# Kernel optimization log

Measured on AMD Instinct MI355X. Metric: run time of the kernel, lower is better.

The kernel has to match this reference:

```python
import jax, jax.numpy as jnp
import numpy as np

TOPK = 13
NUM_CLASSES = 80
ALPHA = 1.0
BETA = 6.0
EPS = 1e-9
CIOU_EPS = 1e-7
IMG = 640
STRIDES = (8, 16, 32)


def _make_anchors():
    anchors = []
    for s in STRIDES:
        n = IMG // s
        xs = (np.arange(n, dtype=np.float32) + 0.5) * s
        gy, gx = np.meshgrid(xs, xs, indexing='ij')
        anchors.append(np.stack([gx.ravel(), gy.ravel()], axis=1))
    return jnp.asarray(np.concatenate(anchors, axis=0))  # (8400, 2)


def setup_inputs() -> dict:
    key = jax.random.key(0)
    k1, k2, k3, k4, k5, k6 = jax.random.split(key, 6)
    B, M, A, C = 16, 64, 8400, 80
    anchor_tensor = _make_anchors()                                   # (A,2)
    pd_scores = jax.random.uniform(k1, (B, A, C), dtype=jnp.float32)  # post-sigmoid scores
    # decoded boxes: anchor +/- positive ltrb distances -> valid x0y0x1y1
    d = jax.random.uniform(k2, (B, A, 4), minval=2.0, maxval=120.0, dtype=jnp.float32)
    anc = anchor_tensor[None]
    pd_boxes = jnp.concatenate([anc - d[..., :2], anc + d[..., 2:]], axis=-1)
    centers = jax.random.uniform(k3, (B, M, 2), minval=16.0, maxval=624.0, dtype=jnp.float32)
    wh = jax.random.uniform(k4, (B, M, 2), minval=8.0, maxval=160.0, dtype=jnp.float32)
    gt_boxes = jnp.concatenate([centers - wh / 2, centers + wh / 2], axis=-1)
    gt_classes = jax.random.randint(k5, (B, M, 1), 0, C, dtype=jnp.int64)
    nvalid = jax.random.randint(k6, (B, 1), 8, M + 1)
    gt_mask = (jnp.arange(M)[None, :] < nvalid)[..., None]            # (B,M,1) bool
    return {"pd_scores": pd_scores, "pd_boxes": pd_boxes, "anchor_tensor": anchor_tensor,
            "gt_classes": gt_classes, "gt_boxes": gt_boxes, "gt_mask": gt_mask}


def boxes_ciou(b1, b2):
    """CIoU between broadcast-compatible x0y0x1y1 boxes; returns same leading shape."""
    b1x1, b1y1, b1x2, b1y2 = b1[..., 0], b1[..., 1], b1[..., 2], b1[..., 3]
    b2x1, b2y1, b2x2, b2y2 = b2[..., 0], b2[..., 1], b2[..., 2], b2[..., 3]
    w1, h1 = b1x2 - b1x1, b1y2 - b1y1 + CIOU_EPS
    w2, h2 = b2x2 - b2x1, b2y2 - b2y1 + CIOU_EPS
    inter = (jnp.minimum(b1x2, b2x2) - jnp.maximum(b1x1, b2x1)).clip(0) * \
            (jnp.minimum(b1y2, b2y2) - jnp.maximum(b1y1, b2y1)).clip(0)
    union = w1 * h1 + w2 * h2 - inter + CIOU_EPS
    iou = inter / union
    cw = jnp.maximum(b1x2, b2x2) - jnp.minimum(b1x1, b2x1)
    ch = jnp.maximum(b1y2, b2y2) - jnp.minimum(b1y1, b2y1)
    c2 = cw * cw + ch * ch + CIOU_EPS
    rho2 = ((b2x1 + b2x2 - b1x1 - b1x2) ** 2 + (b2y1 + b2y2 - b1y1 - b1y2) ** 2) / 4.0
    v = (4.0 / (jnp.pi ** 2)) * (jnp.arctan(w2 / h2) - jnp.arctan(w1 / h1)) ** 2
    alpha = jax.lax.stop_gradient(v / (v - iou + (1.0 + CIOU_EPS)))
    return iou - (rho2 / c2 + v * alpha)


def reference(pd_scores, pd_boxes, anchor_tensor, gt_classes, gt_boxes, gt_mask):
    B, A, C = pd_scores.shape
    M = gt_boxes.shape[1]

    # --- anchors inside GT boxes -> (B, M, A) mask ---
    lt = gt_boxes[:, :, None, :2]                     # (B,M,1,2)
    rb = gt_boxes[:, :, None, 2:]
    anc = anchor_tensor[None, None]                   # (1,1,A,2)
    deltas = jnp.concatenate([anc - lt, rb - anc], axis=-1)   # (B,M,A,4)
    anchors_mask = deltas.min(axis=-1) > 1e-9          # (B,M,A)

    # --- alignment metric ---
    cls = gt_classes[..., 0]                           # (B,M) int
    bi = jnp.arange(B)[:, None, None]
    ai = jnp.arange(A)[None, None, :]
    scores = pd_scores[bi, ai, cls[:, :, None]]        # (B,M,A)
    scores = jnp.where(anchors_mask, scores, 0.0)
    ious = boxes_ciou(gt_boxes[:, :, None, :], pd_boxes[:, None, :, :]).clip(0)
    ious = jnp.where(anchors_mask, ious, 0.0)          # (B,M,A)
    align_metric = scores ** ALPHA * ious ** BETA

    # --- top-k candidate selection with duplicate-count filtering ---
    _, topk_idx = jax.lax.top_k(align_metric, TOPK)    # (B,M,K)
    topk_idx = jnp.where(gt_mask, topk_idx, 0)         # invalid GT -> index 0 (as torch masked_fill)
    mi = jnp.arange(M)[None, :, None]
    counts = jnp.zeros((B, M, A), jnp.int32).at[bi, mi, topk_idx].add(1)
    topk_mask = counts == 1                            # counts>1 zeroed, bool()
    positive_mask = anchors_mask & topk_mask

    # --- filter duplicate anchor assignments (keep highest-IoU GT) ---
    fg = positive_mask.sum(axis=-2)                    # (B,A)
    dup = (fg > 1)[:, None, :]                         # (B,1,A)
    max_iou_idx = jnp.argmax(ious, axis=1)             # (B,A)
    max_iou_mask = jnp.arange(M)[None, :, None] == max_iou_idx[:, None, :]
    positive_mask = jnp.where(dup, max_iou_mask, positive_mask)
    fg = positive_mask.sum(axis=-2)
    target_indices = jnp.argmax(positive_mask, axis=-2)  # (B,A) first-True index
    fg_mask = fg > 0                                     # (B,A) bool

    # --- gather targets ---
    target_boxes = jnp.take_along_axis(gt_boxes, target_indices[:, :, None], axis=1)  # (B,A,4)
    tc = jnp.take_along_axis(cls, target_indices, axis=1).clip(0)                      # (B,A)
    target_scores = jax.nn.one_hot(tc, C, dtype=pd_scores.dtype)
    target_scores = jnp.where(fg_mask[..., None], target_scores, 0.0)

    # --- normalize scores by aligned metric ---
    align_metric = align_metric * positive_mask
    max_align = align_metric.max(axis=-1, keepdims=True)            # (B,M,1)
    max_ious = (ious * positive_mask).max(axis=-1, keepdims=True)   # (B,M,1)
    norm = (align_metric * max_ious / (max_align + EPS)).max(axis=-2)[..., None]  # (B,A,1)
    target_scores = target_scores * norm
    return target_scores, target_boxes, fg_mask
```

## Files before the change

kernel.cpp:

```cpp
#include <hip/hip_runtime.h>
#include <math.h>

#define B_N 16
#define M_N 64
#define A_N 8400
#define C_N 80
#define TOPK_N 13
#define LIST_CAP 640
#define MAIN_CAP (LIST_CAP - TOPK_N)
#define MSK_W 263

__device__ __forceinline__ float2 anchor_xy(int a) {
    int i, j; float s;
    if (a < 6400)      { i = a / 80;            j = a - i * 80; s = 8.f;  }
    else if (a < 8000) { int k = a - 6400; i = k / 40; j = k - i * 40; s = 16.f; }
    else               { int k = a - 8000; i = k / 20; j = k - i * 20; s = 32.f; }
    return make_float2(((float)j + 0.5f) * s, ((float)i + 0.5f) * s);
}

__device__ __forceinline__ float ciou_clip(
    float gx1, float gy1, float gx2, float gy2,
    float w1h1, float atg,
    float px1, float py1, float px2, float py2)
{
    float w2 = px2 - px1;
    float h2 = py2 - py1 + 1e-7f;
    float iw = fminf(gx2, px2) - fmaxf(gx1, px1);
    float ih = fminf(gy2, py2) - fmaxf(gy1, py1);
    float inter = fmaxf(iw, 0.f) * fmaxf(ih, 0.f);
    float uni = w1h1 + w2 * h2 - inter + 1e-7f;
    float iou = inter / uni;
    float cw = fmaxf(gx2, px2) - fminf(gx1, px1);
    float ch = fmaxf(gy2, py2) - fminf(gy1, py1);
    float c2 = cw * cw + ch * ch + 1e-7f;
    float dx = px1 + px2 - gx1 - gx2;
    float dy = py1 + py2 - gy1 - gy2;
    float rho2 = (dx * dx + dy * dy) * 0.25f;
    float dat = atanf(w2 / h2) - atg;
    float v = 0.40528473456935109f * (dat * dat);
    float alpha = v / (v - iou + 1.0000001f);
    return fmaxf(iou - (rho2 / c2 + v * alpha), 0.f);
}

__global__ __launch_bounds__(256) void k_topk(
    const float* __restrict__ pd_scores, const float* __restrict__ pd_boxes,
    const int* __restrict__ gt_classes, const float* __restrict__ gt_boxes,
    const int* __restrict__ gt_mask, unsigned long long* __restrict__ pick)
{
    int bm = blockIdx.x;
    if (!gt_mask[bm]) return;
    int b = bm >> 6, m = bm & 63;
    __shared__ unsigned long long s_list[LIST_CAP];
    __shared__ unsigned int s_msk[MSK_W];
    __shared__ unsigned long long s_key[TOPK_N];
    __shared__ int s_n;
    int tid = threadIdx.x;
    int lane = tid & 63;

    const float* g = gt_boxes + (size_t)bm * 4;
    float gx1 = g[0], gy1 = g[1], gx2 = g[2], gy2 = g[3];
    float w1 = gx2 - gx1, h1 = gy2 - gy1 + 1e-7f;
    float w1h1 = w1 * h1;
    float atg = atanf(w1 / h1);

    if (tid == 0) s_n = 0;
    if (tid < TOPK_N) s_key[tid] = 0ull;
    __syncthreads();

    for (int a = tid; a < A_N; a += 256) {
        float2 an = anchor_xy(a);
        float dmin = fminf(fminf(an.x - gx1, an.y - gy1),
                           fminf(gx2 - an.x, gy2 - an.y));
        bool inb = dmin > 1e-9f;
        unsigned long long mk = __ballot(inb);
        if (lane == 0)       s_msk[a >> 5] = (unsigned int)mk;
        else if (lane == 32) s_msk[a >> 5] = (unsigned int)(mk >> 32);
        if (inb) {
            int ldr = __ffsll(mk) - 1;
            int base = 0;
            if (lane == ldr) base = atomicAdd(&s_n, __popcll(mk));
            base = __shfl(base, ldr, 64);
            int p = base + __popcll(mk & ((1ull << lane) - 1ull));
            if (p < MAIN_CAP)
                s_list[p] = (unsigned long long)(unsigned int)a;
        }
    }
    __syncthreads();

    int n0 = s_n; if (n0 > MAIN_CAP) n0 = MAIN_CAP;
    int cls = gt_classes[bm];
    const float4* pb4 = (const float4*)pd_boxes + (size_t)b * A_N;
    const float* ps = pd_scores + (size_t)b * A_N * C_N + cls;
    for (int p = tid; p < n0; p += 256) {
        int a = (int)(unsigned int)s_list[p];
        float4 pb = pb4[a];
        float io = ciou_clip(gx1, gy1, gx2, gy2, w1h1, atg,
                             pb.x, pb.y, pb.z, pb.w);
        float sc = ps[(size_t)a * C_N];
        float i2 = io * io;
        float al = sc * (i2 * i2 * i2);
        s_list[p] = ((unsigned long long)__float_as_uint(al) << 32)
                  | ((unsigned long long)((unsigned int)(A_N - a) << 1)) | 1ull;
    }
    if (tid == 0) {
        int found = 0;
        for (int wq = 0; wq < MSK_W && found < TOPK_N; ++wq) {
            unsigned int w = ~s_msk[wq];
            if (wq == MSK_W - 1) w &= 0xFFFFu;
            while (w && found < TOPK_N) {
                int bit = __ffs(w) - 1; w &= w - 1;
                int a = wq * 32 + bit;
                s_list[n0 + found] = (unsigned long long)
                                     ((unsigned int)(A_N - a) << 1);
                ++found;
            }
        }
        s_n = n0 + found;
    }
    __syncthreads();
    int n = s_n;

    for (int k = 0; k < TOPK_N; ++k) {
        unsigned long long myb = 0ull; int bp = -1;
        for (int p = tid; p < n; p += 256) {
            unsigned long long t = s_list[p];
            if (t > myb) { myb = t; bp = p; }
        }
        unsigned long long wb = myb;
        for (int off = 32; off > 0; off >>= 1) {
            unsigned long long o = __shfl_xor(wb, off, 64);
            if (o > wb) wb = o;
        }
        if (lane == 0 && wb) atomicMax(&s_key[k], wb);
        __syncthreads();
        unsigned long long win = s_key[k];
        if (myb == win && bp >= 0) {
            s_list[bp] = 0ull;
            if (win & 1ull) {
                int idx = A_N - (int)((win >> 1) & 0x7FFFull);
                atomicOr(&pick[(size_t)b * A_N + idx], 1ull << m);
            }
        }
        __syncthreads();
    }
}

__global__ __launch_bounds__(256) void k_assign(
    const float* __restrict__ pd_scores, const float* __restrict__ pd_boxes,
    const int* __restrict__ gt_classes, const float* __restrict__ gt_boxes,
    const unsigned long long* __restrict__ pick,
    float* __restrict__ out_boxes, float* __restrict__ out_fg,
    int* __restrict__ mtfg, float* __restrict__ alv,
    unsigned int* __restrict__ maxal, unsigned int* __restrict__ maxio)
{
    int i = blockIdx.x * 256 + threadIdx.x;
    if (i >= B_N * A_N) return;
    int b = i / A_N, a = i - b * A_N;
    unsigned long long P = pick[i];
    int fg0 = __popcll(P);
    float2 an = anchor_xy(a);
    float4 pb = ((const float4*)pd_boxes)[i];
    int mt; bool fg;
    if (fg0 > 1) {
        float bestv = -1.f; int bmi = 0;
        for (int mm = 0; mm < M_N; ++mm) {
            const float* g = gt_boxes + ((size_t)b * M_N + mm) * 4;
            float gx1 = g[0], gy1 = g[1], gx2 = g[2], gy2 = g[3];
            float dmin = fminf(fminf(an.x - gx1, an.y - gy1),
                               fminf(gx2 - an.x, gy2 - an.y));
            float v = 0.f;
            if (dmin > 1e-9f) {
                float w1 = gx2 - gx1, h1 = gy2 - gy1 + 1e-7f;
                v = ciou_clip(gx1, gy1, gx2, gy2, w1 * h1, atanf(w1 / h1),
                              pb.x, pb.y, pb.z, pb.w);
            }
            if (v > bestv) { bestv = v; bmi = mm; }
        }
        mt = bmi; fg = true;
    } else {
        fg = (fg0 == 1);
        mt = fg ? (__ffsll(P) - 1) : 0;
    }
    out_fg[i] = fg ? 1.f : 0.f;
    const float* g = gt_boxes + ((size_t)b * M_N + mt) * 4;
    float gx1 = g[0], gy1 = g[1], gx2 = g[2], gy2 = g[3];
    ((float4*)out_boxes)[i] = make_float4(gx1, gy1, gx2, gy2);

    float al = 0.f;
    if (fg) {
        float io = 0.f;
        float dmin = fminf(fminf(an.x - gx1, an.y - gy1),
                           fminf(gx2 - an.x, gy2 - an.y));
        if (dmin > 1e-9f) {
            float w1 = gx2 - gx1, h1 = gy2 - gy1 + 1e-7f;
            io = ciou_clip(gx1, gy1, gx2, gy2, w1 * h1, atanf(w1 / h1),
                           pb.x, pb.y, pb.z, pb.w);
            float sc = pd_scores[(size_t)i * C_N + gt_classes[b * M_N + mt]];
            float i2 = io * io;
            al = sc * (i2 * i2 * i2);
        }
        atomicMax(&maxal[b * M_N + mt], __float_as_uint(al));
        atomicMax(&maxio[b * M_N + mt], __float_as_uint(io));
    }
    mtfg[i] = mt | (fg ? 256 : 0);
    alv[i] = al;
}

#define K3_THREADS (B_N * A_N * (C_N / 4) / 4)
__global__ __launch_bounds__(256) void k_scores(
    const int* __restrict__ mtfg, const float* __restrict__ alv,
    const unsigned int* __restrict__ maxal,
    const unsigned int* __restrict__ maxio,
    const int* __restrict__ gt_classes, float4* __restrict__ out4)
{
    int i0 = blockIdx.x * 256 + threadIdx.x;
    #pragma unroll
    for (int r = 0; r < 4; ++r) {
        int i = i0 + r * K3_THREADS;
        int row = i / (C_N / 4);
        int q = i - row * (C_N / 4);
        int v = mtfg[row];
        float4 o = make_float4(0.f, 0.f, 0.f, 0.f);
        if (v & 256) {
            int mt = v & 255;
            int b = row / A_N;
            int tc = gt_classes[b * M_N + mt];
            if (tc < 0) tc = 0;
            if ((tc >> 2) == q) {
                float al = alv[row];
                float ma = __uint_as_float(maxal[b * M_N + mt]);
                float mi = __uint_as_float(maxio[b * M_N + mt]);
                ((float*)&o)[tc & 3] = al * mi / (ma + 1e-9f);
            }
        }
        out4[i] = o;
    }
}

extern "C" void kernel_launch(void* const* d_in, const int* in_sizes, int n_in,
                              void* d_out, int out_size, void* d_ws, size_t ws_size,
                              hipStream_t stream) {
    const float* pd_scores  = (const float*)d_in[0];
    const float* pd_boxes   = (const float*)d_in[1];
    const int*   gt_classes = (const int*)d_in[3];
    const float* gt_boxes   = (const float*)d_in[4];
    const int*   gt_mask    = (const int*)d_in[5];

    float* out = (float*)d_out;
    float* out_scores = out;
    float* out_boxes  = out + (size_t)B_N * A_N * C_N;
    float* out_fg     = out_boxes + (size_t)B_N * A_N * 4;

    char* w = (char*)d_ws;
    unsigned long long* pick = (unsigned long long*)w; w += (size_t)B_N * A_N * 8;
    unsigned int* maxal = (unsigned int*)w;            w += (size_t)B_N * M_N * 4;
    unsigned int* maxio = (unsigned int*)w;            w += (size_t)B_N * M_N * 4;
    int*   mtfg = (int*)w;                             w += (size_t)B_N * A_N * 4;
    float* alv  = (float*)w;

    hipMemsetAsync(pick, 0,
                   (size_t)B_N * A_N * 8 + (size_t)B_N * M_N * 4 * 2, stream);

    k_topk<<<B_N * M_N, 256, 0, stream>>>(pd_scores, pd_boxes, gt_classes,
                                          gt_boxes, gt_mask, pick);

    int na = (B_N * A_N + 255) / 256;
    k_assign<<<na, 256, 0, stream>>>(pd_scores, pd_boxes, gt_classes,
                                     gt_boxes, pick, out_boxes, out_fg,
                                     mtfg, alv, maxal, maxio);

    k_scores<<<K3_THREADS / 256, 256, 0, stream>>>(mtfg, alv, maxal, maxio,
                                                   gt_classes,
                                                   (float4*)out_scores);
}
```

Before: 154.8 us.

## Replace global pick bitmask and memset with compact top-k lists rebuilt in shared memory

The top-k kernel now writes each GT's 13 selected anchor indices to a small array instead of atomically OR-ing bits into a per-anchor global mask. Each assign block rebuilds its 256-anchor pick masks in shared memory by scanning that batch's lists. Because maxal and maxio are now zeroed inside the top-k kernel, the hipMemsetAsync is gone. This removes a memset launch and about 1 MB of global atomics and traffic, at the cost of every assign block re-reading 832 list entries.

Result: no change. 155.9 us (median of 2 runs) (+0.8%).

```diff
diff --git a/kernel.cpp b/kernel.cpp
--- a/kernel.cpp
+++ b/kernel.cpp
@@ -9,6 +9,7 @@
 #define LIST_CAP 640
 #define MAIN_CAP (LIST_CAP - TOPK_N)
 #define MSK_W 263
+#define ABLK 33
 
 __device__ __forceinline__ float2 anchor_xy(int a) {
     int i, j; float s;
@@ -45,16 +46,18 @@
 __global__ __launch_bounds__(256) void k_topk(
     const float* __restrict__ pd_scores, const float* __restrict__ pd_boxes,
     const int* __restrict__ gt_classes, const float* __restrict__ gt_boxes,
-    const int* __restrict__ gt_mask, unsigned long long* __restrict__ pick)
+    const int* __restrict__ gt_mask, int* __restrict__ topk_out,
+    unsigned int* __restrict__ maxal, unsigned int* __restrict__ maxio)
 {
     int bm = blockIdx.x;
+    int tid = threadIdx.x;
+    if (tid == 0) { maxal[bm] = 0u; maxio[bm] = 0u; }
     if (!gt_mask[bm]) return;
-    int b = bm >> 6, m = bm & 63;
+    int b = bm >> 6;
     __shared__ unsigned long long s_list[LIST_CAP];
     __shared__ unsigned int s_msk[MSK_W];
     __shared__ unsigned long long s_key[TOPK_N];
     __shared__ int s_n;
-    int tid = threadIdx.x;
     int lane = tid & 63;
 
     const float* g = gt_boxes + (size_t)bm * 4;
@@ -136,10 +139,8 @@
         unsigned long long win = s_key[k];
         if (myb == win && bp >= 0) {
             s_list[bp] = 0ull;
-            if (win & 1ull) {
-                int idx = A_N - (int)((win >> 1) & 0x7FFFull);
-                atomicOr(&pick[(size_t)b * A_N + idx], 1ull << m);
-            }
+            int idx = A_N - (int)((win >> 1) & 0x7FFFull);
+            topk_out[bm * TOPK_N + k] = (idx << 1) | (int)(win & 1ull);
         }
         __syncthreads();
     }
@@ -148,15 +149,35 @@
 __global__ __launch_bounds__(256) void k_assign(
     const float* __restrict__ pd_scores, const float* __restrict__ pd_boxes,
     const int* __restrict__ gt_classes, const float* __restrict__ gt_boxes,
-    const unsigned long long* __restrict__ pick,
+    const int* __restrict__ gt_mask, const int* __restrict__ topk_out,
     float* __restrict__ out_boxes, float* __restrict__ out_fg,
     int* __restrict__ mtfg, float* __restrict__ alv,
     unsigned int* __restrict__ maxal, unsigned int* __restrict__ maxio)
 {
-    int i = blockIdx.x * 256 + threadIdx.x;
-    if (i >= B_N * A_N) return;
-    int b = i / A_N, a = i - b * A_N;
-    unsigned long long P = pick[i];
+    __shared__ unsigned long long s_pick[256];
+    int blk = blockIdx.x;
+    int b = blk / ABLK;
+    int a0 = (blk - b * ABLK) * 256;
+    int tid = threadIdx.x;
+    s_pick[tid] = 0ull;
+    __syncthreads();
+    for (int e = tid; e < M_N * TOPK_N; e += 256) {
+        int m = e / TOPK_N;
+        if (gt_mask[b * M_N + m]) {
+            int v = topk_out[b * M_N * TOPK_N + e];
+            if (v & 1) {
+                int idx = (v >> 1) - a0;
+                if ((unsigned)idx < 256u)
+                    atomicOr(&s_pick[idx], 1ull << m);
+            }
+        }
+    }
+    __syncthreads();
+    int a = a0 + tid;
+    if (a >= A_N) return;
+    int i = b * A_N + a;
+
+    unsigned long long P = s_pick[tid];
     int fg0 = __popcll(P);
     float2 an = anchor_xy(a);
     float4 pb = ((const float4*)pd_boxes)[i];
@@ -252,22 +273,21 @@
     float* out_fg     = out_boxes + (size_t)B_N * A_N * 4;
 
     char* w = (char*)d_ws;
-    unsigned long long* pick = (unsigned long long*)w; w += (size_t)B_N * A_N * 8;
-    unsigned int* maxal = (unsigned int*)w;            w += (size_t)B_N * M_N * 4;
-    unsigned int* maxio = (unsigned int*)w;            w += (size_t)B_N * M_N * 4;
-    int*   mtfg = (int*)w;                             w += (size_t)B_N * A_N * 4;
+    int* topk_out = (int*)w;                w += (size_t)B_N * M_N * TOPK_N * 4;
+    unsigned int* maxal = (unsigned int*)w; w += (size_t)B_N * M_N * 4;
+    unsigned int* maxio = (unsigned int*)w; w += (size_t)B_N * M_N * 4;
+    int*   mtfg = (int*)w;                  w += (size_t)B_N * A_N * 4;
     float* alv  = (float*)w;
 
-    hipMemsetAsync(pick, 0,
-                   (size_t)B_N * A_N * 8 + (size_t)B_N * M_N * 4 * 2, stream);
 
     k_topk<<<B_N * M_N, 256, 0, stream>>>(pd_scores, pd_boxes, gt_classes,
-                                          gt_boxes, gt_mask, pick);
-
-    int na = (B_N * A_N + 255) / 256;
-    k_assign<<<na, 256, 0, stream>>>(pd_scores, pd_boxes, gt_classes,
-                                     gt_boxes, pick, out_boxes, out_fg,
-                                     mtfg, alv, maxal, maxio);
+                                          gt_boxes, gt_mask, topk_out,
+                                          maxal, maxio);
+
+    k_assign<<<B_N * ABLK, 256, 0, stream>>>(pd_scores, pd_boxes, gt_classes,
+                                             gt_boxes, gt_mask, topk_out,
+                                             out_boxes, out_fg,
+                                             mtfg, alv, maxal, maxio);
 
     k_scores<<<K3_THREADS / 256, 256, 0, stream>>>(mtfg, alv, maxal, maxio,
                                                    gt_classes,
```
